# Kernel tuning notes

Hardware: AMD Instinct MI355X
Metric: run time of the kernel (lower is better)

Reference implementation:

```python
import jax, jax.numpy as jnp
import numpy as np

B, T, D, H = 8, 2048, 1024, 64

def setup_inputs() -> dict:
    key = jax.random.key(0)
    kx, kq, kk, kv = jax.random.split(key, 4)
    x = jax.random.normal(kx, (B, T, D), dtype=jnp.float32)
    # Linear(embd_size, head_size, bias=False) weights, stored as [D, H] for x @ W
    Wq = jax.random.normal(kq, (D, H), dtype=jnp.float32) * (D ** -0.5)
    Wk = jax.random.normal(kk, (D, H), dtype=jnp.float32) * (D ** -0.5)
    Wv = jax.random.normal(kv, (D, H), dtype=jnp.float32) * (D ** -0.5)
    return {"x": x, "Wq": Wq, "Wk": Wk, "Wv": Wv}

def reference(x, Wq, Wk, Wv):
    Tcur = x.shape[1]
    q = x @ Wq  # [B, T, H]
    k = x @ Wk
    v = x @ Wv
    scores = jnp.einsum('bth,bsh->bts', q, k)
    # NOTE: faithful to source quirk: scores are MULTIPLIED by sqrt(T)
    scores = scores * (Tcur ** 0.5)
    causal = jnp.tril(jnp.ones((Tcur, Tcur), dtype=bool))
    scores = jnp.where(causal, scores, -jnp.inf)
    attn = jax.nn.softmax(scores, axis=2)  # dropout p=0.0 -> identity
    return jnp.einsum('bts,bsh->bth', attn, v)
```

## Files before the change

### kernel.cpp

```cpp
#include <hip/hip_runtime.h>
#include <hip/hip_bf16.h>

#define BB 8
#define TT 2048
#define DD 1024
#define HH 64
#define NROWS (BB*TT)
#define SCALE 45.25483399593904f
#define SPLIT 4
#define BCOLS 320

typedef __attribute__((ext_vector_type(8))) short short8;
typedef __attribute__((ext_vector_type(4))) float f32x4;

__device__ inline ushort bf16rne(float f) {
    unsigned u = __float_as_uint(f);
    return (ushort)((u + 0x7fffu + ((u >> 16) & 1u)) >> 16);
}
__device__ inline void bfsplit(float f, ushort& hi, ushort& lo) {
    hi = bf16rne(f);
    float fh = __uint_as_float(((unsigned)hi) << 16);
    lo = bf16rne(f - fh);
}
__device__ inline void split_pack8(const float* v, int4& h4, int4& l4) {
    ushort h[8], l[8];
    #pragma unroll
    for (int j = 0; j < 8; ++j) bfsplit(v[j], h[j], l[j]);
    h4 = make_int4((int)(h[0] | ((unsigned)h[1] << 16)), (int)(h[2] | ((unsigned)h[3] << 16)),
                   (int)(h[4] | ((unsigned)h[5] << 16)), (int)(h[6] | ((unsigned)h[7] << 16)));
    l4 = make_int4((int)(l[0] | ((unsigned)l[1] << 16)), (int)(l[2] | ((unsigned)l[3] << 16)),
                   (int)(l[4] | ((unsigned)l[5] << 16)), (int)(l[6] | ((unsigned)l[7] << 16)));
}
__device__ inline float bf2f(unsigned u16) {
    return __uint_as_float(u16 << 16);
}

__device__ inline void gload_lds16(const void* g, void* l) {
    __builtin_amdgcn_global_load_lds(
        (const __attribute__((address_space(1))) unsigned int*)(uintptr_t)(g),
        (__attribute__((address_space(3))) unsigned int*)(uintptr_t)(l),
        16, 0, 0);
}

__global__ __launch_bounds__(256) void wprep_kernel(
        const float* __restrict__ Wq, const float* __restrict__ Wk,
        const float* __restrict__ Wv, ushort* __restrict__ Wp) {
    __shared__ float ws[64 * 65];
    const int m = blockIdx.x >> 4;
    const int c = blockIdx.x & 15;
    const float* W = (m == 0) ? Wq : (m == 1) ? Wk : Wv;
    const int tid = threadIdx.x;

    #pragma unroll
    for (int p = 0; p < 4; ++p) {
        int i = tid + p * 256;
        int r = i >> 4, q4 = i & 15;
        float4 v = *(const float4*)(W + (size_t)(c * 64 + r) * 64 + q4 * 4);
        ws[r * 65 + q4 * 4 + 0] = v.x;
        ws[r * 65 + q4 * 4 + 1] = v.y;
        ws[r * 65 + q4 * 4 + 2] = v.z;
        ws[r * 65 + q4 * 4 + 3] = v.w;
    }
    __syncthreads();

    #pragma unroll
    for (int p = 0; p < 2; ++p) {
        int gi = tid + p * 256;
        int nn = gi >> 3, g8 = gi & 7;
        int o  = g8 ^ (nn & 7);
        float v[8];
        #pragma unroll
        for (int j = 0; j < 8; ++j) v[j] = ws[(o * 8 + j) * 65 + nn];
        int4 h4, l4; split_pack8(v, h4, l4);
        const size_t cb = (size_t)c * (BCOLS * 64);
        *(int4*)(Wp + cb + (size_t)(m * 64 + nn) * 64 + g8 * 8) = h4;
        if (m < 2)
            *(int4*)(Wp + cb + (size_t)(192 + m * 64 + nn) * 64 + g8 * 8) = l4;
    }
}

__global__ __launch_bounds__(512) void qkv_kernel(
        const float* __restrict__ x, const ushort* __restrict__ Wp,
        float* __restrict__ Qo, ushort* __restrict__ KhiP,
        ushort* __restrict__ KloP, ushort* __restrict__ VtP) {
    __shared__ ushort Ahi[64 * 64], Alo[64 * 64];
    __shared__ ushort Bp[3][BCOLS * 64];
    const int tid  = threadIdx.x;
    const int lane = tid & 63;
    const int w    = tid >> 6;
    const int wm   = w >> 2;
    const int wn   = w & 3;
    const int n15  = lane & 15;
    const int g    = lane >> 4;
    const int csw  = n15 & 7;
    const int row0 = blockIdx.x * 64;

    f32x4 acc[2][3];
    #pragma unroll
    for (int ms = 0; ms < 2; ++ms)
        #pragma unroll
        for (int nt = 0; nt < 3; ++nt) acc[ms][nt] = (f32x4)0.f;

    const int ar = tid >> 3, aoc = tid & 7;
    const float* xrow = x + (size_t)(row0 + ar) * 1024 + aoc * 8;
    const int adi = ar * 64 + ((aoc ^ (ar & 7)) << 3);

    const ushort* wsp = Wp + (size_t)lane * 8;

    float xA[8], xB[8];
    #pragma unroll
    for (int p = 0; p < 5; ++p) {
        int j = w * 5 + p;
        gload_lds16(wsp + j * 512, &Bp[0][j * 512]);
    }
    *(float4*)(xA)     = *(const float4*)(xrow);
    *(float4*)(xA + 4) = *(const float4*)(xrow + 4);
    #pragma unroll
    for (int p = 0; p < 5; ++p) {
        int j = w * 5 + p;
        gload_lds16(wsp + (size_t)(BCOLS * 64) + j * 512, &Bp[1][j * 512]);
    }
    *(float4*)(xB)     = *(const float4*)(xrow + 64);
    *(float4*)(xB + 4) = *(const float4*)(xrow + 68);

    for (int c = 0; c < 16; ++c) {
        const int cur = c % 3;
        const int c2 = (c + 2 < 16) ? c + 2 : 15;
        {
            const ushort* s = wsp + (size_t)c2 * (BCOLS * 64);
            ushort* d = Bp[(c + 2) % 3];
            #pragma unroll
            for (int p = 0; p < 5; ++p) {
                int j = w * 5 + p;
                gload_lds16(s + j * 512, &d[j * 512]);
            }
        }
        float xN[8];
        {
            const float* src = xrow + (size_t)c2 * 64;
            *(float4*)(xN)     = *(const float4*)(src);
            *(float4*)(xN + 4) = *(const float4*)(src + 4);
        }
        asm volatile("s_waitcnt vmcnt(14)" ::: "memory");
        __builtin_amdgcn_sched_barrier(0);
        {
            int4 h4, l4; split_pack8(xA, h4, l4);
            *(int4*)&Ahi[adi] = h4;
            *(int4*)&Alo[adi] = l4;
        }
        asm volatile("s_waitcnt lgkmcnt(0)" ::: "memory");
        __builtin_amdgcn_s_barrier();
        __builtin_amdgcn_sched_barrier(0);

        #pragma unroll
        for (int kh = 0; kh < 2; ++kh) {
            const int ko = ((4 * kh + g) ^ csw) << 3;
            short8 afh[2], afl[2];
            #pragma unroll
            for (int ms = 0; ms < 2; ++ms) {
                int ao = (wm * 32 + ms * 16 + n15) * 64 + ko;
                afh[ms] = *(const short8*)&Ahi[ao];
                afl[ms] = *(const short8*)&Alo[ao];
            }
            #pragma unroll
            for (int nt = 0; nt < 3; ++nt) {
                const int colb = wn * 48 + nt * 16;
                short8 bfh = *(const short8*)&Bp[cur][(colb + n15) * 64 + ko];
                #pragma unroll
                for (int ms = 0; ms < 2; ++ms) {
                    acc[ms][nt] = __builtin_amdgcn_mfma_f32_16x16x32_bf16(
                        afh[ms], bfh, acc[ms][nt], 0, 0, 0);
                    acc[ms][nt] = __builtin_amdgcn_mfma_f32_16x16x32_bf16(
                        afl[ms], bfh, acc[ms][nt], 0, 0, 0);
                }
                if (colb < 128) {
                    short8 bfl = *(const short8*)&Bp[cur][(192 + colb + n15) * 64 + ko];
                    #pragma unroll
                    for (int ms = 0; ms < 2; ++ms)
                        acc[ms][nt] = __builtin_amdgcn_mfma_f32_16x16x32_bf16(
                            afh[ms], bfl, acc[ms][nt], 0, 0, 0);
                }
            }
        }
        __builtin_amdgcn_s_barrier();
        #pragma unroll
        for (int j = 0; j < 8; ++j) { xA[j] = xB[j]; xB[j] = xN[j]; }
    }

    const int b  = row0 >> 11;
    const int t0 = row0 & 2047;
    #pragma unroll
    for (int nt = 0; nt < 3; ++nt) {
        const int col = wn * 48 + nt * 16 + n15;
        const int mat = col >> 6;
        const int h   = col & 63;
        #pragma unroll
        for (int ms = 0; ms < 2; ++ms) {
            const int mb = row0 + wm * 32 + ms * 16 + 4 * g;
            if (mat == 0) {
                #pragma unroll
                for (int r = 0; r < 4; ++r)
                    Qo[(size_t)(mb + r) * 64 + h] = acc[ms][nt][r];
            } else if (mat == 1) {
                #pragma unroll
                for (int r = 0; r < 4; ++r) {
                    ushort hi, lo; bfsplit(acc[ms][nt][r], hi, lo);
                    KhiP[(size_t)(mb + r) * 64 + h] = hi;
                    KloP[(size_t)(mb + r) * 64 + h] = lo;
                }
            } else {
                ushort pk[4];
                #pragma unroll
                for (int r = 0; r < 4; ++r) pk[r] = bf16rne(acc[ms][nt][r]);
                const int tloc = t0 + wm * 32 + ms * 16 + 4 * g;
                *(uint2*)&VtP[((size_t)(b * 64 + h)) * 2048 + tloc] =
                    make_uint2(pk[0] | ((unsigned)pk[1] << 16),
                               pk[2] | ((unsigned)pk[3] << 16));
            }
        }
    }
}

__global__ __launch_bounds__(128) void attn_kernel(
        const float* __restrict__ Q, const ushort* __restrict__ Khi,
        const ushort* __restrict__ Klo, const ushort* __restrict__ Vt,
        ushort* __restrict__ PaccH, float* __restrict__ Pm,
        float* __restrict__ Pl) {
    __shared__ ushort KhiL[64 * 64];
    __shared__ ushort KloL[64 * 64];
    __shared__ ushort VtL[64 * 64];
    const int tid  = threadIdx.x;
    const int lane = tid & 63;
    const int w    = tid >> 6;
    const int n    = lane & 15;
    const int g    = lane >> 4;
    const int b    = blockIdx.y;
    const int xx   = blockIdx.x;
    const int qt   = 63 - (xx >> 2);
    const int sp   = xx & 3;
    const int q0   = qt * 32;
    const int qmin = q0 + w * 16;
    const int qrow = qmin + n;
    const int csw  = n & 7;
    const int ntiles = (q0 >> 6) + 1;
    const int it0  = (ntiles * sp) >> 2;
    const int it1  = (ntiles * (sp + 1)) >> 2;

    short8 qhi0, qhi1, qlo0, qlo1;
    {
        const float* qp = Q + ((size_t)b * TT + qrow) * HH + 8 * g;
        float v0[8], v1[8];
        *(float4*)(v0)     = *(const float4*)(qp);
        *(float4*)(v0 + 4) = *(const float4*)(qp + 4);
        *(float4*)(v1)     = *(const float4*)(qp + 32);
        *(float4*)(v1 + 4) = *(const float4*)(qp + 36);
        #pragma unroll
        for (int j = 0; j < 8; ++j) {
            ushort hi, lo;
            bfsplit(v0[j], hi, lo); qhi0[j] = (short)hi; qlo0[j] = (short)lo;
            bfsplit(v1[j], hi, lo); qhi1[j] = (short)hi; qlo1[j] = (short)lo;
        }
    }

    f32x4 accO[4];
    #pragma unroll
    for (int t = 0; t < 4; ++t) accO[t] = (f32x4)0.f;
    float m = -1e30f, l = 0.f;

    const ushort* gkh = Khi + (size_t)b * TT * HH;
    const ushort* gkl = Klo + (size_t)b * TT * HH;
    const ushort* gvt = Vt + (size_t)b * 64 * TT;

    const int crow = lane >> 3;
    const int coct = lane & 7;

    for (int it = it0; it < it1; ++it) {
        const int kb = it * 64;
        __syncthreads();
        #pragma unroll
        for (int p = 0; p < 4; ++p) {
            const int cc  = w * 4 + p;
            const int row = (cc << 3) + crow;
            const int soc = coct ^ (row & 7);
            gload_lds16(gkh + (size_t)(kb + row) * HH + (soc << 3), &KhiL[cc << 9]);
            gload_lds16(gkl + (size_t)(kb + row) * HH + (soc << 3), &KloL[cc << 9]);
            gload_lds16(gvt + (size_t)row * TT + kb + (soc << 3),   &VtL[cc << 9]);
        }
        __syncthreads();

        f32x4 s4[4];
        #pragma unroll
        for (int s = 0; s < 4; ++s) {
            const int keyl = 16 * s + n;
            const ushort* kbase = &KhiL[keyl << 6];
            const ushort* lbase = &KloL[keyl << 6];
            short8 kh0 = *(const short8*)(kbase + ((g ^ csw) << 3));
            short8 kh1 = *(const short8*)(kbase + (((4 + g) ^ csw) << 3));
            short8 kl0 = *(const short8*)(lbase + ((g ^ csw) << 3));
            short8 kl1 = *(const short8*)(lbase + (((4 + g) ^ csw) << 3));
            f32x4 a = (f32x4)0.f;
            a = __builtin_amdgcn_mfma_f32_16x16x32_bf16(kh0, qhi0, a, 0, 0, 0);
            a = __builtin_amdgcn_mfma_f32_16x16x32_bf16(kh1, qhi1, a, 0, 0, 0);
            a = __builtin_amdgcn_mfma_f32_16x16x32_bf16(kl0, qhi0, a, 0, 0, 0);
            a = __builtin_amdgcn_mfma_f32_16x16x32_bf16(kl1, qhi1, a, 0, 0, 0);
            a = __builtin_amdgcn_mfma_f32_16x16x32_bf16(kh0, qlo0, a, 0, 0, 0);
            a = __builtin_amdgcn_mfma_f32_16x16x32_bf16(kh1, qlo1, a, 0, 0, 0);
            s4[s] = a;
        }

        float sm[16];
        if (kb + 63 > qmin) {
            #pragma unroll
            for (int s = 0; s < 4; ++s)
                #pragma unroll
                for (int r = 0; r < 4; ++r) {
                    int keyg = kb + 16 * s + 4 * g + r;
                    sm[s * 4 + r] = (keyg <= qrow) ? s4[s][r] * SCALE : -1e30f;
                }
        } else {
            #pragma unroll
            for (int s = 0; s < 4; ++s)
                #pragma unroll
                for (int r = 0; r < 4; ++r) sm[s * 4 + r] = s4[s][r] * SCALE;
        }
        float pm = sm[0];
        #pragma unroll
        for (int i = 1; i < 16; ++i) pm = fmaxf(pm, sm[i]);
        pm = fmaxf(pm, __shfl_xor(pm, 16));
        pm = fmaxf(pm, __shfl_xor(pm, 32));
        float mn = fmaxf(m, pm);
        float es = __expf(m - mn);
        float p[16], ps = 0.f;
        #pragma unroll
        for (int i = 0; i < 16; ++i) { p[i] = __expf(sm[i] - mn); ps += p[i]; }
        ps += __shfl_xor(ps, 16);
        ps += __shfl_xor(ps, 32);
        l = l * es + ps;
        m = mn;
        #pragma unroll
        for (int t = 0; t < 4; ++t)
            #pragma unroll
            for (int r = 0; r < 4; ++r) accO[t][r] *= es;

        short8 pf0, pf1;
        #pragma unroll
        for (int j = 0; j < 4; ++j) {
            pf0[j]     = (short)bf16rne(p[0 * 4 + j]);
            pf0[j + 4] = (short)bf16rne(p[1 * 4 + j]);
            pf1[j]     = (short)bf16rne(p[2 * 4 + j]);
            pf1[j + 4] = (short)bf16rne(p[3 * 4 + j]);
        }

        #pragma unroll
        for (int t = 0; t < 4; ++t) {
            const int h = 16 * t + n;
            const ushort* vb = &VtL[h << 6];
            union { int2 d[2]; short8 v; } u0, u1;
            u0.d[0] = *(const int2*)(vb + ((4 * g) ^ (csw << 3)));
            u0.d[1] = *(const int2*)(vb + ((16 + 4 * g) ^ (csw << 3)));
            u1.d[0] = *(const int2*)(vb + ((32 + 4 * g) ^ (csw << 3)));
            u1.d[1] = *(const int2*)(vb + ((48 + 4 * g) ^ (csw << 3)));
            accO[t] = __builtin_amdgcn_mfma_f32_16x16x32_bf16(u0.v, pf0, accO[t], 0, 0, 0);
            accO[t] = __builtin_amdgcn_mfma_f32_16x16x32_bf16(u1.v, pf1, accO[t], 0, 0, 0);
        }
    }

    const size_t brow = (size_t)b * TT + qrow;
    ushort* pa = PaccH + ((size_t)sp * NROWS + brow) * 64 + 4 * g;
    #pragma unroll
    for (int t = 0; t < 4; ++t) {
        ushort e0 = bf16rne(accO[t][0]), e1 = bf16rne(accO[t][1]);
        ushort e2 = bf16rne(accO[t][2]), e3 = bf16rne(accO[t][3]);
        *(uint2*)(pa + 16 * t) = make_uint2(e0 | ((unsigned)e1 << 16),
                                            e2 | ((unsigned)e3 << 16));
    }
    if (g == 0) {
        Pm[(size_t)sp * NROWS + brow] = m;
        Pl[(size_t)sp * NROWS + brow] = l;
    }
}

__global__ __launch_bounds__(256) void combine_kernel(
        const ushort* __restrict__ PaccH, const float* __restrict__ Pm,
        const float* __restrict__ Pl, float* __restrict__ out) {
    const int u    = blockIdx.x * 256 + threadIdx.x;
    const int row  = u >> 2;
    const int quad = u & 3;

    float ms[SPLIT], ls[SPLIT], M = -1e30f;
    #pragma unroll
    for (int s = 0; s < SPLIT; ++s) {
        ms[s] = Pm[(size_t)s * NROWS + row];
        ls[s] = Pl[(size_t)s * NROWS + row];
        M = fmaxf(M, ms[s]);
    }
    float wgt[SPLIT], den = 0.f;
    #pragma unroll
    for (int s = 0; s < SPLIT; ++s) {
        wgt[s] = __expf(ms[s] - M);
        den += wgt[s] * ls[s];
    }
    const float inv = 1.0f / den;

    float4 o[4];
    #pragma unroll
    for (int i = 0; i < 4; ++i) o[i] = make_float4(0.f, 0.f, 0.f, 0.f);
    #pragma unroll
    for (int s = 0; s < SPLIT; ++s) {
        const ushort* a = PaccH + ((size_t)s * NROWS + row) * 64 + quad * 16;
        #pragma unroll
        for (int i = 0; i < 4; ++i) {
            uint2 uv = *(const uint2*)(a + i * 4);
            o[i].x += wgt[s] * bf2f(uv.x & 0xffffu);
            o[i].y += wgt[s] * bf2f(uv.x >> 16);
            o[i].z += wgt[s] * bf2f(uv.y & 0xffffu);
            o[i].w += wgt[s] * bf2f(uv.y >> 16);
        }
    }
    float4* op = (float4*)(out + (size_t)row * 64 + quad * 16);
    #pragma unroll
    for (int i = 0; i < 4; ++i)
        op[i] = make_float4(o[i].x * inv, o[i].y * inv, o[i].z * inv, o[i].w * inv);
}

extern "C" void kernel_launch(void* const* d_in, const int* in_sizes, int n_in,
                              void* d_out, int out_size, void* d_ws, size_t ws_size,
                              hipStream_t stream) {
    const float* x  = (const float*)d_in[0];
    const float* Wq = (const float*)d_in[1];
    const float* Wk = (const float*)d_in[2];
    const float* Wv = (const float*)d_in[3];
    float* outp = (float*)d_out;

    float*  Qw    = (float*)d_ws;
    ushort* KhiP  = (ushort*)(Qw + (size_t)NROWS * HH);
    ushort* KloP  = KhiP + (size_t)NROWS * HH;
    ushort* VtP   = KloP + (size_t)NROWS * HH;
    ushort* Wp    = VtP + (size_t)NROWS * HH;
    ushort* PaccH = Wp + (size_t)16 * BCOLS * 64;
    float*  Pm    = (float*)(PaccH + (size_t)SPLIT * NROWS * HH);
    float*  Pl    = Pm + (size_t)SPLIT * NROWS;

    wprep_kernel<<<48, 256, 0, stream>>>(Wq, Wk, Wv, Wp);
    qkv_kernel<<<NROWS / 64, 512, 0, stream>>>(x, Wp, Qw, KhiP, KloP, VtP);
    attn_kernel<<<dim3(64 * SPLIT, BB), 128, 0, stream>>>(Qw, KhiP, KloP, VtP,
                                                          PaccH, Pm, Pl);
    combine_kernel<<<NROWS * 4 / 256, 256, 0, stream>>>(PaccH, Pm, Pl, outp);
}
```

Before: 68.27 us.

## Double-buffer K/V LDS tiles with async prefetch of next key block

Turns the single LDS buffer for Khi/Klo/Vt into a ping-pong pair and issues the direct-to-LDS global loads for the next key tile before computing the current one. Explicit vmcnt waits and raw s_barrier replace the two __syncthreads per iteration, so load latency can overlap the MFMA and softmax work. The cost is doubled LDS use (48 KB per block), which may lower occupancy, plus reliance on hand-counted vmcnt values that must match the compiler's actual load count.

Result: slower. 73.08 us (+7.1%).

```diff
diff --git a/kernel.cpp b/kernel.cpp
--- a/kernel.cpp
+++ b/kernel.cpp
@@ -226,9 +226,9 @@
         const ushort* __restrict__ Klo, const ushort* __restrict__ Vt,
         ushort* __restrict__ PaccH, float* __restrict__ Pm,
         float* __restrict__ Pl) {
-    __shared__ ushort KhiL[64 * 64];
-    __shared__ ushort KloL[64 * 64];
-    __shared__ ushort VtL[64 * 64];
+    __shared__ ushort KhiL[2][64 * 64];
+    __shared__ ushort KloL[2][64 * 64];
+    __shared__ ushort VtL[2][64 * 64];
     const int tid  = threadIdx.x;
     const int lane = tid & 63;
     const int w    = tid >> 6;
@@ -274,94 +274,117 @@
     const int crow = lane >> 3;
     const int coct = lane & 7;
 
-    for (int it = it0; it < it1; ++it) {
-        const int kb = it * 64;
-        __syncthreads();
-        #pragma unroll
-        for (int p = 0; p < 4; ++p) {
-            const int cc  = w * 4 + p;
-            const int row = (cc << 3) + crow;
-            const int soc = coct ^ (row & 7);
-            gload_lds16(gkh + (size_t)(kb + row) * HH + (soc << 3), &KhiL[cc << 9]);
-            gload_lds16(gkl + (size_t)(kb + row) * HH + (soc << 3), &KloL[cc << 9]);
-            gload_lds16(gvt + (size_t)row * TT + kb + (soc << 3),   &VtL[cc << 9]);
-        }
-        __syncthreads();
-
-        f32x4 s4[4];
-        #pragma unroll
-        for (int s = 0; s < 4; ++s) {
-            const int keyl = 16 * s + n;
-            const ushort* kbase = &KhiL[keyl << 6];
-            const ushort* lbase = &KloL[keyl << 6];
-            short8 kh0 = *(const short8*)(kbase + ((g ^ csw) << 3));
-            short8 kh1 = *(const short8*)(kbase + (((4 + g) ^ csw) << 3));
-            short8 kl0 = *(const short8*)(lbase + ((g ^ csw) << 3));
-            short8 kl1 = *(const short8*)(lbase + (((4 + g) ^ csw) << 3));
-            f32x4 a = (f32x4)0.f;
-            a = __builtin_amdgcn_mfma_f32_16x16x32_bf16(kh0, qhi0, a, 0, 0, 0);
-            a = __builtin_amdgcn_mfma_f32_16x16x32_bf16(kh1, qhi1, a, 0, 0, 0);
-            a = __builtin_amdgcn_mfma_f32_16x16x32_bf16(kl0, qhi0, a, 0, 0, 0);
-            a = __builtin_amdgcn_mfma_f32_16x16x32_bf16(kl1, qhi1, a, 0, 0, 0);
-            a = __builtin_amdgcn_mfma_f32_16x16x32_bf16(kh0, qlo0, a, 0, 0, 0);
-            a = __builtin_amdgcn_mfma_f32_16x16x32_bf16(kh1, qlo1, a, 0, 0, 0);
-            s4[s] = a;
-        }
-
-        float sm[16];
-        if (kb + 63 > qmin) {
-            #pragma unroll
-            for (int s = 0; s < 4; ++s)
-                #pragma unroll
-                for (int r = 0; r < 4; ++r) {
-                    int keyg = kb + 16 * s + 4 * g + r;
-                    sm[s * 4 + r] = (keyg <= qrow) ? s4[s][r] * SCALE : -1e30f;
+    if (it0 < it1) {
+        {
+            const int kb = it0 * 64;
+            #pragma unroll
+            for (int p = 0; p < 4; ++p) {
+                const int cc  = w * 4 + p;
+                const int row = (cc << 3) + crow;
+                const int soc = coct ^ (row & 7);
+                gload_lds16(gkh + (size_t)(kb + row) * HH + (soc << 3), &KhiL[0][cc << 9]);
+                gload_lds16(gkl + (size_t)(kb + row) * HH + (soc << 3), &KloL[0][cc << 9]);
+                gload_lds16(gvt + (size_t)row * TT + kb + (soc << 3),   &VtL[0][cc << 9]);
+            }
+        }
+
+        for (int it = it0; it < it1; ++it) {
+            const int kb = it * 64;
+            const int li = (it - it0) & 1;
+            if (it + 1 < it1) {
+                const int nb = (it + 1) * 64;
+                #pragma unroll
+                for (int p = 0; p < 4; ++p) {
+                    const int cc  = w * 4 + p;
+                    const int row = (cc << 3) + crow;
+                    const int soc = coct ^ (row & 7);
+                    gload_lds16(gkh + (size_t)(nb + row) * HH + (soc << 3), &KhiL[li ^ 1][cc << 9]);
+                    gload_lds16(gkl + (size_t)(nb + row) * HH + (soc << 3), &KloL[li ^ 1][cc << 9]);
+                    gload_lds16(gvt + (size_t)row * TT + nb + (soc << 3),   &VtL[li ^ 1][cc << 9]);
                 }
-        } else {
-            #pragma unroll
-            for (int s = 0; s < 4; ++s)
-                #pragma unroll
-                for (int r = 0; r < 4; ++r) sm[s * 4 + r] = s4[s][r] * SCALE;
-        }
-        float pm = sm[0];
-        #pragma unroll
-        for (int i = 1; i < 16; ++i) pm = fmaxf(pm, sm[i]);
-        pm = fmaxf(pm, __shfl_xor(pm, 16));
-        pm = fmaxf(pm, __shfl_xor(pm, 32));
-        float mn = fmaxf(m, pm);
-        float es = __expf(m - mn);
-        float p[16], ps = 0.f;
-        #pragma unroll
-        for (int i = 0; i < 16; ++i) { p[i] = __expf(sm[i] - mn); ps += p[i]; }
-        ps += __shfl_xor(ps, 16);
-        ps += __shfl_xor(ps, 32);
-        l = l * es + ps;
-        m = mn;
-        #pragma unroll
-        for (int t = 0; t < 4; ++t)
-            #pragma unroll
-            for (int r = 0; r < 4; ++r) accO[t][r] *= es;
-
-        short8 pf0, pf1;
-        #pragma unroll
-        for (int j = 0; j < 4; ++j) {
-            pf0[j]     = (short)bf16rne(p[0 * 4 + j]);
-            pf0[j + 4] = (short)bf16rne(p[1 * 4 + j]);
-            pf1[j]     = (short)bf16rne(p[2 * 4 + j]);
-            pf1[j + 4] = (short)bf16rne(p[3 * 4 + j]);
-        }
-
-        #pragma unroll
-        for (int t = 0; t < 4; ++t) {
-            const int h = 16 * t + n;
-            const ushort* vb = &VtL[h << 6];
-            union { int2 d[2]; short8 v; } u0, u1;
-            u0.d[0] = *(const int2*)(vb + ((4 * g) ^ (csw << 3)));
-            u0.d[1] = *(const int2*)(vb + ((16 + 4 * g) ^ (csw << 3)));
-            u1.d[0] = *(const int2*)(vb + ((32 + 4 * g) ^ (csw << 3)));
-            u1.d[1] = *(const int2*)(vb + ((48 + 4 * g) ^ (csw << 3)));
-            accO[t] = __builtin_amdgcn_mfma_f32_16x16x32_bf16(u0.v, pf0, accO[t], 0, 0, 0);
-            accO[t] = __builtin_amdgcn_mfma_f32_16x16x32_bf16(u1.v, pf1, accO[t], 0, 0, 0);
+                asm volatile("s_waitcnt vmcnt(12)" ::: "memory");
+            } else {
+                asm volatile("s_waitcnt vmcnt(0)" ::: "memory");
+            }
+            __builtin_amdgcn_s_barrier();
+            __builtin_amdgcn_sched_barrier(0);
+
+            f32x4 s4[4];
+            #pragma unroll
+            for (int s = 0; s < 4; ++s) {
+                const int keyl = 16 * s + n;
+                const ushort* kbase = &KhiL[li][keyl << 6];
+                const ushort* lbase = &KloL[li][keyl << 6];
+                short8 kh0 = *(const short8*)(kbase + ((g ^ csw) << 3));
+                short8 kh1 = *(const short8*)(kbase + (((4 + g) ^ csw) << 3));
+                short8 kl0 = *(const short8*)(lbase + ((g ^ csw) << 3));
+                short8 kl1 = *(const short8*)(lbase + (((4 + g) ^ csw) << 3));
+                f32x4 a = (f32x4)0.f;
+                a = __builtin_amdgcn_mfma_f32_16x16x32_bf16(kh0, qhi0, a, 0, 0, 0);
+                a = __builtin_amdgcn_mfma_f32_16x16x32_bf16(kh1, qhi1, a, 0, 0, 0);
+                a = __builtin_amdgcn_mfma_f32_16x16x32_bf16(kl0, qhi0, a, 0, 0, 0);
+                a = __builtin_amdgcn_mfma_f32_16x16x32_bf16(kl1, qhi1, a, 0, 0, 0);
+                a = __builtin_amdgcn_mfma_f32_16x16x32_bf16(kh0, qlo0, a, 0, 0, 0);
+                a = __builtin_amdgcn_mfma_f32_16x16x32_bf16(kh1, qlo1, a, 0, 0, 0);
+                s4[s] = a;
+            }
+
+            float sm[16];
+            if (kb + 63 > qmin) {
+                #pragma unroll
+                for (int s = 0; s < 4; ++s)
+                    #pragma unroll
+                    for (int r = 0; r < 4; ++r) {
+                        int keyg = kb + 16 * s + 4 * g + r;
+                        sm[s * 4 + r] = (keyg <= qrow) ? s4[s][r] * SCALE : -1e30f;
+                    }
+            } else {
+                #pragma unroll
+                for (int s = 0; s < 4; ++s)
+                    #pragma unroll
+                    for (int r = 0; r < 4; ++r) sm[s * 4 + r] = s4[s][r] * SCALE;
+            }
+            float pm = sm[0];
+            #pragma unroll
+            for (int i = 1; i < 16; ++i) pm = fmaxf(pm, sm[i]);
+            pm = fmaxf(pm, __shfl_xor(pm, 16));
+            pm = fmaxf(pm, __shfl_xor(pm, 32));
+            float mn = fmaxf(m, pm);
+            float es = __expf(m - mn);
+            float p[16], ps = 0.f;
+            #pragma unroll
+            for (int i = 0; i < 16; ++i) { p[i] = __expf(sm[i] - mn); ps += p[i]; }
+            ps += __shfl_xor(ps, 16);
+            ps += __shfl_xor(ps, 32);
+            l = l * es + ps;
+            m = mn;
+            #pragma unroll
+            for (int t = 0; t < 4; ++t)
+                #pragma unroll
+                for (int r = 0; r < 4; ++r) accO[t][r] *= es;
+
+            short8 pf0, pf1;
+            #pragma unroll
+            for (int j = 0; j < 4; ++j) {
+                pf0[j]     = (short)bf16rne(p[0 * 4 + j]);
+                pf0[j + 4] = (short)bf16rne(p[1 * 4 + j]);
+                pf1[j]     = (short)bf16rne(p[2 * 4 + j]);
+                pf1[j + 4] = (short)bf16rne(p[3 * 4 + j]);
+            }
+
+            #pragma unroll
+            for (int t = 0; t < 4; ++t) {
+                const int h = 16 * t + n;
+                const ushort* vb = &VtL[li][h << 6];
+                union { int2 d[2]; short8 v; } u0, u1;
+                u0.d[0] = *(const int2*)(vb + ((4 * g) ^ (csw << 3)));
+                u0.d[1] = *(const int2*)(vb + ((16 + 4 * g) ^ (csw << 3)));
+                u1.d[0] = *(const int2*)(vb + ((32 + 4 * g) ^ (csw << 3)));
+                u1.d[1] = *(const int2*)(vb + ((48 + 4 * g) ^ (csw << 3)));
+                accO[t] = __builtin_amdgcn_mfma_f32_16x16x32_bf16(u0.v, pf0, accO[t], 0, 0, 0);
+                accO[t] = __builtin_amdgcn_mfma_f32_16x16x32_bf16(u1.v, pf1, accO[t], 0, 0, 0);
+            }
+            __builtin_amdgcn_s_barrier();
         }
     }
 
```
